# Kernel tuning notes

Hardware: AMD Instinct MI355X
Metric: run time of the kernel (lower is better)

Reference implementation:

```python
import jax, jax.numpy as jnp
import numpy as np

N_NODES = 100000
N_EDGES = 800000

def setup_inputs() -> dict:
    key = jax.random.key(0)
    ks = jax.random.split(key, 8)
    x = jax.random.normal(ks[0], (N_NODES, 500), dtype=jnp.float32)
    edge_index = jax.random.randint(ks[1], (2, N_EDGES), 0, N_NODES, dtype=jnp.int64)
    s = lambda k, shape, fan_in: jax.random.normal(k, shape, jnp.float32) / np.sqrt(fan_in)
    return {
        "x": x,
        "edge_index": edge_index,
        "W1_l": s(ks[2], (500, 20), 500),
        "W1_r": s(ks[3], (500, 20), 500),
        "b1": jnp.zeros((20,), jnp.float32),
        "W2_l": s(ks[4], (20, 3), 20),
        "W2_r": s(ks[5], (20, 3), 20),
        "b2": jnp.zeros((3,), jnp.float32),
    }

def _sage_conv(x, src, dst, W_l, W_r, b, deg_inv):
    # mean-aggregate neighbor features (x_j = x[src]) at dst, PyG default 'mean'
    agg = jax.ops.segment_sum(x[src], dst, num_segments=x.shape[0])  # [N, F]
    agg = agg * deg_inv[:, None]
    return agg @ W_l + b + x @ W_r

def reference(x, edge_index, W1_l, W1_r, b1, W2_l, W2_r, b2):
    src, dst = edge_index[0], edge_index[1]
    deg = jax.ops.segment_sum(jnp.ones_like(dst, dtype=x.dtype), dst, num_segments=x.shape[0])
    deg_inv = 1.0 / jnp.maximum(deg, 1.0)
    h = _sage_conv(x, src, dst, W1_l, W1_r, b1, deg_inv)
    h = jax.nn.relu(h)
    # F.dropout(p=0.5, training=self.training): identity in eval mode
    out = _sage_conv(h, src, dst, W2_l, W2_r, b2, deg_inv)
    return out
```

## Files before the change

kernel.cpp:

```cpp
#include <hip/hip_runtime.h>

#define F_IN  500
#define F_HID 20
#define F_OUT 3
#define KT    16
#define NT    3
#define PAD   64

typedef __attribute__((ext_vector_type(8))) short short8;
typedef __attribute__((ext_vector_type(4))) float v4f;

__device__ __forceinline__ unsigned f2bf(float f) {
    unsigned u = __float_as_uint(f);
    u = u + 0x7fffu + ((u >> 16) & 1u);
    return u >> 16;
}
__device__ __forceinline__ float bf2f(unsigned h) {
    return __uint_as_float(h << 16);
}

__device__ __forceinline__ void cvt8(const float4 p, const float4 q, short8& hi, short8& lo) {
    float vf[8] = {p.x, p.y, p.z, p.w, q.x, q.y, q.z, q.w};
    union { unsigned u[4]; short8 s; } H, L;
#pragma unroll
    for (int t = 0; t < 4; ++t) {
        unsigned u0 = __float_as_uint(vf[2*t]);
        unsigned u1 = __float_as_uint(vf[2*t+1]);
        unsigned r0 = u0 + 0x7fffu + ((u0 >> 16) & 1u);
        unsigned r1 = u1 + 0x7fffu + ((u1 >> 16) & 1u);
        float f0 = __uint_as_float(r0 & 0xffff0000u);
        float f1 = __uint_as_float(r1 & 0xffff0000u);
        float d0 = vf[2*t]   - f0;
        float d1 = vf[2*t+1] - f1;
        unsigned s0 = __float_as_uint(d0); s0 = s0 + 0x7fffu + ((s0 >> 16) & 1u);
        unsigned s1 = __float_as_uint(d1); s1 = s1 + 0x7fffu + ((s1 >> 16) & 1u);
        H.u[t] = (r0 >> 16) | (r1 & 0xffff0000u);
        L.u[t] = (s0 >> 16) | (s1 & 0xffff0000u);
    }
    hi = H.s; lo = L.s;
}

__global__ void k_init(const float* __restrict__ W1l, const float* __restrict__ W1r,
                       unsigned short* __restrict__ Bhi, unsigned short* __restrict__ Blo,
                       int* __restrict__ deg, int NZ4) {
    int b = blockIdx.x;
    int tid = threadIdx.x;
    if (b < (KT * NT * 64) / 256) {
        int i = b * 256 + tid;
        int lane = i & 63;
        int ntk  = i >> 6;
        int nt   = ntk % NT;
        int kt   = ntk / NT;
        int n     = nt * 16 + (lane & 15);
        int kbase = kt * 32 + (lane >> 4) * 8;
#pragma unroll
        for (int j = 0; j < 8; ++j) {
            int k = kbase + j;
            float w = 0.f;
            if (k < F_IN && n < 2 * F_HID)
                w = (n < F_HID) ? W1l[k * F_HID + n] : W1r[k * F_HID + (n - F_HID)];
            unsigned h = f2bf(w);
            Bhi[(size_t)i * 8 + j] = (unsigned short)h;
            Blo[(size_t)i * 8 + j] = (unsigned short)f2bf(w - bf2f(h));
        }
    } else {
        int i = (b - (KT * NT * 64) / 256) * 256 + tid;
        if (i < NZ4) ((int4*)deg)[i] = make_int4(0, 0, 0, 0);
    }
}

__global__ __launch_bounds__(256, 3) void k_gemm_fill(const float* __restrict__ x,
        const unsigned short* __restrict__ Bhi, const unsigned short* __restrict__ Blo,
        float* __restrict__ yl, float* __restrict__ yr,
        const int* __restrict__ src, const int* __restrict__ dst,
        int* __restrict__ deg, int* __restrict__ csr,
        int N, int E, int GB) {
    if ((int)blockIdx.x >= GB) {
        int e = ((int)blockIdx.x - GB) * 256 + (int)threadIdx.x;
        if (e < E) {
            int dn = dst[e];
            int pos = atomicAdd(&deg[dn], 1);
            if (pos < PAD) csr[(size_t)dn * PAD + pos] = src[e];
        }
        return;
    }
    const int lane = threadIdx.x & 63;
    const int wv   = threadIdx.x >> 6;
    const int fr   = lane & 15;
    const int kq   = lane >> 4;
    const int rowA = blockIdx.x * 128 + wv * 32;

    const int r0 = min(rowA + fr,      N - 1);
    const int r1 = min(rowA + 16 + fr, N - 1);
    const float* __restrict__ xp0 = x + (size_t)r0 * F_IN;
    const float* __restrict__ xp1 = x + (size_t)r1 * F_IN;

    v4f acc[2][NT];
#pragma unroll
    for (int h = 0; h < 2; ++h)
#pragma unroll
        for (int nt = 0; nt < NT; ++nt)
            acc[h][nt] = (v4f){0.f, 0.f, 0.f, 0.f};

    float4 xb[2][4];
    short8 bh[2][NT], bl[2][NT];
    {
        const int kb = kq * 8;
        xb[0][0] = *(const float4*)(xp0 + kb);
        xb[0][1] = *(const float4*)(xp0 + kb + 4);
        xb[0][2] = *(const float4*)(xp1 + kb);
        xb[0][3] = *(const float4*)(xp1 + kb + 4);
#pragma unroll
        for (int nt = 0; nt < NT; ++nt) {
            size_t fo = ((size_t)nt * 64 + lane) * 8;
            bh[0][nt] = *(const short8*)(Bhi + fo);
            bl[0][nt] = *(const short8*)(Blo + fo);
        }
    }
#pragma unroll
    for (int kt = 0; kt < KT; ++kt) {
        const int cb = kt & 1, nb = cb ^ 1;
        if (kt + 1 < KT) {
            const int kb = (kt + 1) * 32 + kq * 8;
            const int ka = (kb     <= 496) ? kb     : 496;
            const int kc = (kb + 4 <= 496) ? kb + 4 : 496;
            xb[nb][0] = *(const float4*)(xp0 + ka);
            xb[nb][1] = *(const float4*)(xp0 + kc);
            xb[nb][2] = *(const float4*)(xp1 + ka);
            xb[nb][3] = *(const float4*)(xp1 + kc);
#pragma unroll
            for (int nt = 0; nt < NT; ++nt) {
                size_t fo = (((size_t)(kt + 1) * NT + nt) * 64 + lane) * 8;
                bh[nb][nt] = *(const short8*)(Bhi + fo);
                bl[nb][nt] = *(const short8*)(Blo + fo);
            }
        }
        short8 Ah0, Al0, Ah1, Al1;
        cvt8(xb[cb][0], xb[cb][1], Ah0, Al0);
        cvt8(xb[cb][2], xb[cb][3], Ah1, Al1);
#pragma unroll
        for (int nt = 0; nt < NT; ++nt) {
            acc[0][nt] = __builtin_amdgcn_mfma_f32_16x16x32_bf16(Ah0, bh[cb][nt], acc[0][nt], 0, 0, 0);
            acc[0][nt] = __builtin_amdgcn_mfma_f32_16x16x32_bf16(Ah0, bl[cb][nt], acc[0][nt], 0, 0, 0);
            acc[0][nt] = __builtin_amdgcn_mfma_f32_16x16x32_bf16(Al0, bh[cb][nt], acc[0][nt], 0, 0, 0);
            acc[1][nt] = __builtin_amdgcn_mfma_f32_16x16x32_bf16(Ah1, bh[cb][nt], acc[1][nt], 0, 0, 0);
            acc[1][nt] = __builtin_amdgcn_mfma_f32_16x16x32_bf16(Ah1, bl[cb][nt], acc[1][nt], 0, 0, 0);
            acc[1][nt] = __builtin_amdgcn_mfma_f32_16x16x32_bf16(Al1, bh[cb][nt], acc[1][nt], 0, 0, 0);
        }
    }
#pragma unroll
    for (int h = 0; h < 2; ++h) {
        int rbase = rowA + h * 16 + kq * 4;
#pragma unroll
        for (int nt = 0; nt < NT; ++nt) {
            int col = nt * 16 + fr;
            if (col < 2 * F_HID) {
#pragma unroll
                for (int rg = 0; rg < 4; ++rg) {
                    int grow = rbase + rg;
                    if (grow < N) {
                        if (col < F_HID) yl[(size_t)grow * 32 + col] = acc[h][nt][rg];
                        else             yr[(size_t)grow * F_HID + (col - F_HID)] = acc[h][nt][rg];
                    }
                }
            }
        }
    }
}

__global__ __launch_bounds__(256) void k_agg_l1(
        const int* __restrict__ deg, const int* __restrict__ csr,
        const float* __restrict__ yl, const float* __restrict__ yr,
        const float* __restrict__ b1, const float* __restrict__ W2l,
        const float* __restrict__ W2r,
        float* __restrict__ zl4, float* __restrict__ zr, int N) {
    int t = blockIdx.x * blockDim.x + threadIdx.x;
    int n = t >> 3;
    int g = t & 7;
    if (n >= N) return;
    int d   = min(deg[n], PAD);
    size_t beg = (size_t)n * PAD;
    float4 a = make_float4(0.f, 0.f, 0.f, 0.f);
    if (g < 5) {
        int j = 0;
        for (; j + 1 < d; j += 2) {
            int s0 = csr[beg + j];
            int s1 = csr[beg + j + 1];
            float4 v0 = *(const float4*)(yl + (size_t)s0 * 32 + g * 4);
            float4 v1 = *(const float4*)(yl + (size_t)s1 * 32 + g * 4);
            a.x += v0.x; a.y += v0.y; a.z += v0.z; a.w += v0.w;
            a.x += v1.x; a.y += v1.y; a.z += v1.z; a.w += v1.w;
        }
        if (j < d) {
            int s0 = csr[beg + j];
            float4 v0 = *(const float4*)(yl + (size_t)s0 * 32 + g * 4);
            a.x += v0.x; a.y += v0.y; a.z += v0.z; a.w += v0.w;
        }
    }
    float di = 1.0f / fmaxf((float)d, 1.0f);
    float pl0 = 0.f, pl1 = 0.f, pl2 = 0.f, pr0 = 0.f, pr1 = 0.f, pr2 = 0.f;
    if (g < 5) {
        float4 bb = *(const float4*)(b1 + g * 4);
        float4 rr = *(const float4*)(yr + (size_t)n * F_HID + g * 4);
        float h0 = fmaxf(a.x * di + bb.x + rr.x, 0.f);
        float h1 = fmaxf(a.y * di + bb.y + rr.y, 0.f);
        float h2 = fmaxf(a.z * di + bb.z + rr.z, 0.f);
        float h3 = fmaxf(a.w * di + bb.w + rr.w, 0.f);
        const float* wl = W2l + g * 4 * F_OUT;
        const float* wr = W2r + g * 4 * F_OUT;
        pl0 = h0 * wl[0] + h1 * wl[3] + h2 * wl[6] + h3 * wl[9];
        pl1 = h0 * wl[1] + h1 * wl[4] + h2 * wl[7] + h3 * wl[10];
        pl2 = h0 * wl[2] + h1 * wl[5] + h2 * wl[8] + h3 * wl[11];
        pr0 = h0 * wr[0] + h1 * wr[3] + h2 * wr[6] + h3 * wr[9];
        pr1 = h0 * wr[1] + h1 * wr[4] + h2 * wr[7] + h3 * wr[10];
        pr2 = h0 * wr[2] + h1 * wr[5] + h2 * wr[8] + h3 * wr[11];
    }
#pragma unroll
    for (int m = 4; m >= 1; m >>= 1) {
        pl0 += __shfl_xor(pl0, m);
        pl1 += __shfl_xor(pl1, m);
        pl2 += __shfl_xor(pl2, m);
        pr0 += __shfl_xor(pr0, m);
        pr1 += __shfl_xor(pr1, m);
        pr2 += __shfl_xor(pr2, m);
    }
    if (g == 0) {
        *(float4*)(zl4 + (size_t)n * 4) = make_float4(pl0, pl1, pl2, 0.f);
        zr[(size_t)n * 3 + 0] = pr0;
        zr[(size_t)n * 3 + 1] = pr1;
        zr[(size_t)n * 3 + 2] = pr2;
    }
}

__global__ void k_agg2_final(const int* __restrict__ deg, const int* __restrict__ csr,
                             const float* __restrict__ zl4, const float* __restrict__ zr,
                             const float* __restrict__ b2, float* __restrict__ out, int N) {
    int n = blockIdx.x * blockDim.x + threadIdx.x;
    if (n >= N) return;
    int d   = min(deg[n], PAD);
    size_t beg = (size_t)n * PAD;
    float a0 = 0.f, a1 = 0.f, a2 = 0.f;
    int j = 0;
    for (; j + 1 < d; j += 2) {
        int s0 = csr[beg + j];
        int s1 = csr[beg + j + 1];
        float4 z0 = *(const float4*)(zl4 + (size_t)s0 * 4);
        float4 z1 = *(const float4*)(zl4 + (size_t)s1 * 4);
        a0 += z0.x; a1 += z0.y; a2 += z0.z;
        a0 += z1.x; a1 += z1.y; a2 += z1.z;
    }
    if (j < d) {
        int s0 = csr[beg + j];
        float4 z0 = *(const float4*)(zl4 + (size_t)s0 * 4);
        a0 += z0.x; a1 += z0.y; a2 += z0.z;
    }
    float di = 1.0f / fmaxf((float)d, 1.0f);
    out[(size_t)n * F_OUT + 0] = a0 * di + b2[0] + zr[(size_t)n * 3 + 0];
    out[(size_t)n * F_OUT + 1] = a1 * di + b2[1] + zr[(size_t)n * 3 + 1];
    out[(size_t)n * F_OUT + 2] = a2 * di + b2[2] + zr[(size_t)n * 3 + 2];
}

extern "C" void kernel_launch(void* const* d_in, const int* in_sizes, int n_in,
                              void* d_out, int out_size, void* d_ws, size_t ws_size,
                              hipStream_t stream) {
    const float* x   = (const float*)d_in[0];
    const int*   ei  = (const int*)d_in[1];
    const float* W1l = (const float*)d_in[2];
    const float* W1r = (const float*)d_in[3];
    const float* b1  = (const float*)d_in[4];
    const float* W2l = (const float*)d_in[5];
    const float* W2r = (const float*)d_in[6];
    const float* b2  = (const float*)d_in[7];
    float* out = (float*)d_out;

    const int N = in_sizes[0] / F_IN;
    const int E = in_sizes[1] / 2;
    const int* src = ei;
    const int* dst = ei + E;

    int*   wsi  = (int*)d_ws;
    int*   deg  = wsi;
    int*   csr  = deg + ((N + 3) & ~3);
    float* yl   = (float*)(csr + (size_t)N * PAD);
    float* yr   = yl + (size_t)N * 32;
    float* zl4  = yr + (size_t)N * F_HID;
    float* zr   = zl4 + (size_t)N * 4;
    unsigned short* Bhi = (unsigned short*)(zr + (size_t)N * F_OUT + 1);
    unsigned short* Blo = Bhi + (size_t)KT * NT * 64 * 8;

    const int B   = 256;
    const int PB  = (KT * NT * 64) / B;
    const int NZ4 = (N + 3) / 4;
    const int ZB  = (NZ4 + B - 1) / B;
    const int GB  = (N + 127) / 128;
    const int FB  = (E + B - 1) / B;

    k_init      <<<PB + ZB, B, 0, stream>>>(W1l, W1r, Bhi, Blo, deg, NZ4);
    k_gemm_fill <<<GB + FB, B, 0, stream>>>(x, Bhi, Blo, yl, yr, src, dst, deg, csr, N, E, GB);
    k_agg_l1    <<<((size_t)N * 8 + B - 1) / B, B, 0, stream>>>(deg, csr, yl, yr, b1, W2l, W2r, zl4, zr, N);
    k_agg2_final<<<(N + B - 1) / B, B, 0, stream>>>(deg, csr, zl4, zr, b2, out, N);
}
```

Baseline: 385.9 us.

## Shrink GEMM wave tile to 16 rows and drop manual double buffering

```diff
diff --git a/kernel.cpp b/kernel.cpp
--- a/kernel.cpp
+++ b/kernel.cpp
@@ -69,7 +69,7 @@
     }
 }
 
-__global__ __launch_bounds__(256, 3) void k_gemm_fill(const float* __restrict__ x,
+__global__ __launch_bounds__(256) void k_gemm_fill(const float* __restrict__ x,
         const unsigned short* __restrict__ Bhi, const unsigned short* __restrict__ Blo,
         float* __restrict__ yl, float* __restrict__ yr,
         const int* __restrict__ src, const int* __restrict__ dst,
@@ -88,80 +88,45 @@
     const int wv   = threadIdx.x >> 6;
     const int fr   = lane & 15;
     const int kq   = lane >> 4;
-    const int rowA = blockIdx.x * 128 + wv * 32;
-
-    const int r0 = min(rowA + fr,      N - 1);
-    const int r1 = min(rowA + 16 + fr, N - 1);
+    const int rowA = blockIdx.x * 64 + wv * 16;
+
+    const int r0 = min(rowA + fr, N - 1);
     const float* __restrict__ xp0 = x + (size_t)r0 * F_IN;
-    const float* __restrict__ xp1 = x + (size_t)r1 * F_IN;
-
-    v4f acc[2][NT];
-#pragma unroll
-    for (int h = 0; h < 2; ++h)
-#pragma unroll
-        for (int nt = 0; nt < NT; ++nt)
-            acc[h][nt] = (v4f){0.f, 0.f, 0.f, 0.f};
-
-    float4 xb[2][4];
-    short8 bh[2][NT], bl[2][NT];
-    {
-        const int kb = kq * 8;
-        xb[0][0] = *(const float4*)(xp0 + kb);
-        xb[0][1] = *(const float4*)(xp0 + kb + 4);
-        xb[0][2] = *(const float4*)(xp1 + kb);
-        xb[0][3] = *(const float4*)(xp1 + kb + 4);
+
+    v4f acc[NT];
+#pragma unroll
+    for (int nt = 0; nt < NT; ++nt) acc[nt] = (v4f){0.f, 0.f, 0.f, 0.f};
+
+#pragma unroll 2
+    for (int kt = 0; kt < KT; ++kt) {
+        const int kb = kt * 32 + kq * 8;
+        const int ka = (kb     <= 496) ? kb     : 496;
+        const int kc = (kb + 4 <= 496) ? kb + 4 : 496;
+        float4 a0 = *(const float4*)(xp0 + ka);
+        float4 a1 = *(const float4*)(xp0 + kc);
+        short8 Ah, Al;
+        cvt8(a0, a1, Ah, Al);
 #pragma unroll
         for (int nt = 0; nt < NT; ++nt) {
-            size_t fo = ((size_t)nt * 64 + lane) * 8;
-            bh[0][nt] = *(const short8*)(Bhi + fo);
-            bl[0][nt] = *(const short8*)(Blo + fo);
-        }
-    }
-#pragma unroll
-    for (int kt = 0; kt < KT; ++kt) {
-        const int cb = kt & 1, nb = cb ^ 1;
-        if (kt + 1 < KT) {
-            const int kb = (kt + 1) * 32 + kq * 8;
-            const int ka = (kb     <= 496) ? kb     : 496;
-            const int kc = (kb + 4 <= 496) ? kb + 4 : 496;
-            xb[nb][0] = *(const float4*)(xp0 + ka);
-            xb[nb][1] = *(const float4*)(xp0 + kc);
-            xb[nb][2] = *(const float4*)(xp1 + ka);
-            xb[nb][3] = *(const float4*)(xp1 + kc);
-#pragma unroll
-            for (int nt = 0; nt < NT; ++nt) {
-                size_t fo = (((size_t)(kt + 1) * NT + nt) * 64 + lane) * 8;
-                bh[nb][nt] = *(const short8*)(Bhi + fo);
-                bl[nb][nt] = *(const short8*)(Blo + fo);
-            }
-        }
-        short8 Ah0, Al0, Ah1, Al1;
-        cvt8(xb[cb][0], xb[cb][1], Ah0, Al0);
-        cvt8(xb[cb][2], xb[cb][3], Ah1, Al1);
-#pragma unroll
-        for (int nt = 0; nt < NT; ++nt) {
-            acc[0][nt] = __builtin_amdgcn_mfma_f32_16x16x32_bf16(Ah0, bh[cb][nt], acc[0][nt], 0, 0, 0);
-            acc[0][nt] = __builtin_amdgcn_mfma_f32_16x16x32_bf16(Ah0, bl[cb][nt], acc[0][nt], 0, 0, 0);
-            acc[0][nt] = __builtin_amdgcn_mfma_f32_16x16x32_bf16(Al0, bh[cb][nt], acc[0][nt], 0, 0, 0);
-            acc[1][nt] = __builtin_amdgcn_mfma_f32_16x16x32_bf16(Ah1, bh[cb][nt], acc[1][nt], 0, 0, 0);
-            acc[1][nt] = __builtin_amdgcn_mfma_f32_16x16x32_bf16(Ah1, bl[cb][nt], acc[1][nt], 0, 0, 0);
-            acc[1][nt] = __builtin_amdgcn_mfma_f32_16x16x32_bf16(Al1, bh[cb][nt], acc[1][nt], 0, 0, 0);
-        }
-    }
-#pragma unroll
-    for (int h = 0; h < 2; ++h) {
-        int rbase = rowA + h * 16 + kq * 4;
-#pragma unroll
-        for (int nt = 0; nt < NT; ++nt) {
-            int col = nt * 16 + fr;
-            if (col < 2 * F_HID) {
-#pragma unroll
-                for (int rg = 0; rg < 4; ++rg) {
-                    int grow = rbase + rg;
-                    if (grow < N) {
-                        if (col < F_HID) yl[(size_t)grow * 32 + col] = acc[h][nt][rg];
-                        else             yr[(size_t)grow * F_HID + (col - F_HID)] = acc[h][nt][rg];
-                    }
+            size_t fo = (((size_t)kt * NT + nt) * 64 + lane) * 8;
+            short8 Bh = *(const short8*)(Bhi + fo);
+            short8 Bl = *(const short8*)(Blo + fo);
+            acc[nt] = __builtin_amdgcn_mfma_f32_16x16x32_bf16(Ah, Bh, acc[nt], 0, 0, 0);
+            acc[nt] = __builtin_amdgcn_mfma_f32_16x16x32_bf16(Ah, Bl, acc[nt], 0, 0, 0);
+            acc[nt] = __builtin_amdgcn_mfma_f32_16x16x32_bf16(Al, Bh, acc[nt], 0, 0, 0);
+        }
+    }
+    int rbase = rowA + kq * 4;
+#pragma unroll
+    for (int nt = 0; nt < NT; ++nt) {
+        int col = nt * 16 + fr;
+        if (col < 2 * F_HID) {
+#pragma unroll
+            for (int rg = 0; rg < 4; ++rg) {
+                int grow = rbase + rg;
+                if (grow < N) {
+                    if (col < F_HID) yl[(size_t)grow * 32 + col] = acc[nt][rg];
+                    else             yr[(size_t)grow * F_HID + (col - F_HID)] = acc[nt][rg];
                 }
             }
         }
@@ -292,7 +257,7 @@
     const int PB  = (KT * NT * 64) / B;
     const int NZ4 = (N + 3) / 4;
     const int ZB  = (NZ4 + B - 1) / B;
-    const int GB  = (N + 127) / 128;
+    const int GB  = (N + 63) / 64;
     const int FB  = (E + B - 1) / B;
 
     k_init      <<<PB + ZB, B, 0, stream>>>(W1l, W1r, Bhi, Blo, deg, NZ4);
```

Result: no change. 392.3 us (+1.7%).
